# Kernel optimization log

Measured on AMD Instinct MI355X. Metric: run time of the kernel, lower is better.

The kernel has to match this reference:

```python
import jax, jax.numpy as jnp
import numpy as np

N = 100000      # nodes
E = 1600000     # directed edges
F_IN = 128      # node feature dim
H = 128         # hidden dim
C = 16          # classes


def setup_inputs() -> dict:
    key = jax.random.key(0)
    ks = jax.random.split(key, 8)
    s = 1.0 / np.sqrt(H)
    return {
        "x": jax.random.normal(ks[0], (N, F_IN), dtype=jnp.float32),
        "edge_index": jax.random.randint(ks[1], (2, E), 0, N, dtype=jnp.int32),
        "W1": jax.random.normal(ks[2], (F_IN, H), dtype=jnp.float32) * s,
        "b1": jnp.zeros((H,), jnp.float32),
        "W2": jax.random.normal(ks[3], (H, H), dtype=jnp.float32) * s,
        "b2": jnp.zeros((H,), jnp.float32),
        "W3": jax.random.normal(ks[4], (H, H), dtype=jnp.float32) * s,
        "b3": jnp.zeros((H,), jnp.float32),
        "Wfc": jax.random.normal(ks[5], (H, C), dtype=jnp.float32) * s,
        "bfc": jnp.zeros((C,), jnp.float32),
    }


def _gcn_conv(x, W, b, src, dst, norm):
    # x' = b + scatter_add over edges of norm * (x @ W)[src] into dst
    h = x @ W                                   # [N, H] dense GEMM
    msg = h[src] * norm[:, None]                # [E+N, H] gather + scale
    out = jax.ops.segment_sum(msg, dst, num_segments=N)  # scatter-add
    return out + b


def reference(x, edge_index, W1, b1, W2, b2, W3, b3, Wfc, bfc):
    loops = jnp.arange(N, dtype=edge_index.dtype)
    src = jnp.concatenate([edge_index[0], loops])   # [E+N] with self-loops
    dst = jnp.concatenate([edge_index[1], loops])
    # symmetric normalization deg^{-1/2}[src] * deg^{-1/2}[dst] (PyG default)
    deg = jax.ops.segment_sum(jnp.ones_like(dst, dtype=x.dtype), dst, num_segments=N)
    dinv = jax.lax.rsqrt(deg)                       # deg >= 1 due to self-loops
    norm = dinv[src] * dinv[dst]

    h = jax.nn.elu(_gcn_conv(x, W1, b1, src, dst, norm))   # dropout is identity in eval
    h = jax.nn.elu(_gcn_conv(h, W2, b2, src, dst, norm))
    h = jax.nn.elu(_gcn_conv(h, W3, b3, src, dst, norm))
    logits = h @ Wfc + bfc                                  # [N, C]
    return jax.nn.log_softmax(logits, axis=-1)
```

## Files before the change

kernel.cpp:

```cpp
#include <hip/hip_runtime.h>
#include <math.h>

#define HDIM 128
#define CDIM 16
#define CAP 48
#define ASTR 136
#define HSTR 132
#define NBINS 256
#define TILE 4096
#define NPBMAX 512
#define SORTCAP 7424

typedef unsigned short u16;
typedef unsigned int u32;
typedef __attribute__((ext_vector_type(8))) short short8;
typedef __attribute__((ext_vector_type(4))) float f32x4;
typedef __attribute__((ext_vector_type(2))) float f32x2;

__device__ inline u16 f2bf(float f) {
  u32 u = __float_as_uint(f);
  u += 0x7fffu + ((u >> 16) & 1u);
  return (u16)(u >> 16);
}
__device__ inline float bf_lo(u32 p) { return __uint_as_float(p << 16); }
__device__ inline float bf_hi(u32 p) { return __uint_as_float(p & 0xffff0000u); }
__device__ inline u32 cvtpk(float a, float b) {
  u32 r;
  asm("v_cvt_pk_bf16_f32 %0, %1, %2" : "=v"(r) : "v"(a), "v"(b));
  return r;
}
__device__ inline void acc_word(f32x2& acc, u32 w) {
  f32x2 x;
  x.x = __uint_as_float(w << 16);
  x.y = __uint_as_float(w & 0xffff0000u);
  asm("v_pk_add_f32 %0, %1, %2" : "=v"(acc) : "v"(x), "v"(acc));
}


__global__ __launch_bounds__(256) void bin_kernel(const int* __restrict__ ei,
                                                  int* __restrict__ cursor,
                                                  u32* __restrict__ bins,
                                                  int binCap, int E, int npb, int nbE,
                                                  int nbW, int N,
                                                  const float* __restrict__ W0,
                                                  const float* __restrict__ W1,
                                                  const float* __restrict__ W2,
                                                  u16* __restrict__ Wt,
                                                  u16* __restrict__ Arow,
                                                  u16* __restrict__ Brow,
                                                  u16* __restrict__ Xrow) {
  int tid = threadIdx.x;
  if (blockIdx.x >= nbE) {
    if (blockIdx.x >= nbE + nbW) {
      if (tid < 16) ((uint4*)Arow)[tid] = make_uint4(0, 0, 0, 0);
      else if (tid < 32) ((uint4*)Brow)[tid - 16] = make_uint4(0, 0, 0, 0);
      else if (tid < 48) ((uint4*)Xrow)[tid - 32] = make_uint4(0, 0, 0, 0);
      return;
    }
    int t = (blockIdx.x - nbE) * 256 + tid;
    int which = t >> 14, idx = t & 16383;
    int n = idx >> 7, k = idx & 127;
    const float* W = which == 0 ? W0 : (which == 1 ? W1 : W2);
    Wt[(size_t)which * HDIM * HDIM + n * HDIM + k] = f2bf(W[k * HDIM + n]);
    return;
  }
  __shared__ u32 eds32[TILE];
  __shared__ u32 srt[TILE];
  __shared__ unsigned char bid[TILE];
  __shared__ int hist[NBINS], lbase[NBINS + 1], gbase[NBINS], rnk[NBINS];
  int t0 = blockIdx.x * TILE;
  int n = min(TILE, E - t0);
  hist[tid] = 0;
  rnk[tid] = 0;
  __syncthreads();
  for (int i = tid; i < n; i += 256) {
    int s = ei[t0 + i];
    int d = ei[E + t0 + i];
    int b = d / npb;
    eds32[i] = ((u32)(d - b * npb) << 17) | (u32)s;
    bid[i] = (unsigned char)b;
    atomicAdd(&hist[b], 1);
  }
  __syncthreads();
  int h = hist[tid];
  lbase[tid] = h;
  __syncthreads();
#pragma unroll
  for (int off = 1; off < 256; off <<= 1) {
    int v = tid >= off ? lbase[tid - off] : 0;
    __syncthreads();
    lbase[tid] += v;
    __syncthreads();
  }
  int ex = lbase[tid] - h;
  __syncthreads();
  lbase[tid] = ex;
  if (tid == 255) lbase[256] = ex + h;
  gbase[tid] = h ? atomicAdd(&cursor[tid], h) : 0;
  __syncthreads();
  for (int i = tid; i < n; i += 256) {
    int b = bid[i];
    int r = lbase[b] + atomicAdd(&rnk[b], 1);
    srt[r] = eds32[i];
  }
  __syncthreads();
  for (int i = tid; i < n; i += 256) {
    int lo = 0, hi = 255;
#pragma unroll
    for (int k = 0; k < 8; ++k) {
      int mid = (lo + hi + 1) >> 1;
      if (lbase[mid] <= i) lo = mid; else hi = mid - 1;
    }
    int r = gbase[lo] + (i - lbase[lo]);
    if (r < binCap) bins[(size_t)lo * binCap + r] = srt[i];
  }
}

__global__ __launch_bounds__(256) void fill2_kernel(const u32* __restrict__ bins,
                                                    const int* __restrict__ cursor,
                                                    int binCap, int npb,
                                                    int* __restrict__ deg,
                                                    int* __restrict__ csr, int N) {
  __shared__ int hist[NPBMAX];
  __shared__ int base[NPBMAX + 1];
  __shared__ int sorted[SORTCAP];
  int b = blockIdx.x;
  int tid = threadIdx.x;
  int n0 = b * npb;
  int nn = min(npb, N - n0);
  if (nn <= 0) return;
  int cnt = min(min(cursor[b], binCap), SORTCAP);
  const u32* eb = bins + (size_t)b * binCap;
  for (int i = tid; i < nn; i += 256) hist[i] = 0;
  __syncthreads();
  for (int i = tid; i < cnt; i += 256) atomicAdd(&hist[eb[i] >> 17], 1);
  __syncthreads();
  if (tid == 0) {
    int s = 0;
    for (int i = 0; i < nn; ++i) { base[i] = s; s += hist[i]; }
    base[nn] = s;
  }
  __syncthreads();
  for (int i = tid; i < nn; i += 256) hist[i] = 0;
  __syncthreads();
  for (int i = tid; i < cnt; i += 256) {
    u32 w = eb[i];
    int loc = w >> 17;
    sorted[base[loc] + atomicAdd(&hist[loc], 1)] = (int)(w & 0x1FFFFu);
  }
  __syncthreads();
  for (int i = tid; i < nn; i += 256) deg[n0 + i] = base[i + 1] - base[i];
  int total = nn * CAP;
  int* cout = csr + (size_t)n0 * CAP;
  for (int i = tid; i < total; i += 256) {
    int loc = (int)(((u32)(i >> 4) * 21846u) >> 16);
    int j = i - loc * CAP;
    int s0 = base[loc];
    int dc = min(base[loc + 1] - s0, CAP);
    cout[i] = j < dc ? sorted[s0 + j] : N;
  }
}

__global__ __launch_bounds__(256) void convert_k(const float* __restrict__ x,
                                                 const int* __restrict__ deg,
                                                 u16* __restrict__ Xc, int N) {
  int rg = blockIdx.x * 64 + (threadIdx.x >> 2);
  if (rg >= N) return;
  int c = threadIdx.x & 3;
  float dv = rsqrtf((float)(deg[rg] + 1));
  const float4* src = (const float4*)(x + (size_t)rg * HDIM + c * 32);
  uint4* dst = (uint4*)(Xc + (size_t)rg * HDIM + c * 32);
#pragma unroll
  for (int j = 0; j < 4; ++j) {
    float4 a = src[2 * j], b = src[2 * j + 1];
    uint4 o;
    o.x = cvtpk(dv * a.x, dv * a.y); o.y = cvtpk(dv * a.z, dv * a.w);
    o.z = cvtpk(dv * b.x, dv * b.y); o.w = cvtpk(dv * b.z, dv * b.w);
    dst[j] = o;
  }
}


__device__ inline void gather16(const u16* __restrict__ G, const int* __restrict__ deg,
                                const int* __restrict__ csr, int node, int l, float* v) {
  const char* Gb = (const char*)G;
  f32x2 p0, p1, p2, p3;
  {
    uint4 sr = *(const uint4*)(Gb + ((size_t)node << 8) + (l << 4));
    p0.x = bf_lo(sr.x); p0.y = bf_hi(sr.x);
    p1.x = bf_lo(sr.y); p1.y = bf_hi(sr.y);
    p2.x = bf_lo(sr.z); p2.y = bf_hi(sr.z);
    p3.x = bf_lo(sr.w); p3.y = bf_hi(sr.w);
  }
  int dfull = deg[node];
  int d = min(dfull, CAP);
  int dp = (d + 7) & ~7;
  const int* row = csr + (size_t)node * CAP;
  int i0 = row[l];
  int i1 = d > 16 ? row[16 + l] : 0;
  int i2 = d > 32 ? row[32 + l] : 0;

#define GLD(u) (*(const uint4*)(Gb + (((u32)(u)) << 8) + (l << 4)))
#define AW(gv) { acc_word(p0, gv.x); acc_word(p1, gv.y); acc_word(p2, gv.z); acc_word(p3, gv.w); }
  for (int k = 0; k < dp; k += 8) {
    int s = k < 16 ? i0 : (k < 32 ? i1 : i2);
    int bl = k & 15;
    int u0 = __shfl(s, bl + 0, 16), u1 = __shfl(s, bl + 1, 16);
    int u2 = __shfl(s, bl + 2, 16), u3 = __shfl(s, bl + 3, 16);
    int u4 = __shfl(s, bl + 4, 16), u5 = __shfl(s, bl + 5, 16);
    int u6 = __shfl(s, bl + 6, 16), u7 = __shfl(s, bl + 7, 16);
    uint4 g0 = GLD(u0), g1 = GLD(u1), g2 = GLD(u2), g3 = GLD(u3);
    uint4 g4 = GLD(u4), g5 = GLD(u5), g6 = GLD(u6), g7 = GLD(u7);
    AW(g0) AW(g1) AW(g2) AW(g3) AW(g4) AW(g5) AW(g6) AW(g7)
  }
#undef AW
#undef GLD
  float dvn = rsqrtf((float)(dfull + 1));
  v[0] = dvn * p0.x; v[1] = dvn * p0.y;
  v[2] = dvn * p1.x; v[3] = dvn * p1.y;
  v[4] = dvn * p2.x; v[5] = dvn * p2.y;
  v[6] = dvn * p3.x; v[7] = dvn * p3.y;
}


__global__ __launch_bounds__(256) void agg_gemm(const u16* __restrict__ G,
                                                const int* __restrict__ deg,
                                                const int* __restrict__ csr,
                                                const float* __restrict__ b,
                                                const u16* __restrict__ Wn,
                                                u16* __restrict__ Gout, int N) {
  __shared__ u16 As[16 * ASTR];
  __shared__ float dvs[16];
  int tid = threadIdx.x;
  int node0 = blockIdx.x * 16;
  int lr = tid >> 4, l = tid & 15;
  int node = node0 + lr;
  if (tid < 16) dvs[tid] = rsqrtf((float)(deg[min(node0 + tid, N - 1)] + 1));
  if (node < N) {
    float v[8];
    gather16(G, deg, csr, node, l, v);
    uint4 o;
    o.x = cvtpk(v[0], v[1]); o.y = cvtpk(v[2], v[3]);
    o.z = cvtpk(v[4], v[5]); o.w = cvtpk(v[6], v[7]);
    *(uint4*)(As + lr * ASTR + l * 8) = o;
  } else {
    *(uint4*)(As + lr * ASTR + l * 8) = make_uint4(0, 0, 0, 0);
  }
  __syncthreads();

  int w = tid >> 6;
  int lw = tid & 63;
  int m = lw & 15, q = lw >> 4;
  f32x4 acc0 = (f32x4){0.f, 0.f, 0.f, 0.f};
  f32x4 acc1 = (f32x4){0.f, 0.f, 0.f, 0.f};
#pragma unroll
  for (int kc = 0; kc < 4; ++kc) {
    short8 af = *(const short8*)(As + m * ASTR + kc * 32 + q * 8);
    short8 b0 = *(const short8*)(Wn + ((w * 2 + 0) * 16 + m) * HDIM + kc * 32 + q * 8);
    short8 b1 = *(const short8*)(Wn + ((w * 2 + 1) * 16 + m) * HDIM + kc * 32 + q * 8);
    acc0 = __builtin_amdgcn_mfma_f32_16x16x32_bf16(af, b0, acc0, 0, 0, 0);
    acc1 = __builtin_amdgcn_mfma_f32_16x16x32_bf16(af, b1, acc1, 0, 0, 0);
  }
  __syncthreads();

  float bc0 = b[(w * 2 + 0) * 16 + m], bc1 = b[(w * 2 + 1) * 16 + m];
#pragma unroll
  for (int r = 0; r < 4; ++r) {
    float dvr = dvs[q * 4 + r];
    float h0 = acc0[r] + bc0; h0 = h0 > 0.f ? h0 : __expf(h0) - 1.f;
    float h1 = acc1[r] + bc1; h1 = h1 > 0.f ? h1 : __expf(h1) - 1.f;
    As[(q * 4 + r) * ASTR + (w * 2 + 0) * 16 + m] = f2bf(h0 * dvr);
    As[(q * 4 + r) * ASTR + (w * 2 + 1) * 16 + m] = f2bf(h1 * dvr);
  }
  __syncthreads();

  {
    int r = tid >> 4, c = tid & 15;
    if (node0 + r < N)
      *(uint4*)(Gout + (size_t)(node0 + r) * HDIM + c * 8) =
          *(const uint4*)(As + r * ASTR + c * 8);
  }
}


__global__ __launch_bounds__(256) void agg_fc(const u16* __restrict__ G,
                                              const int* __restrict__ deg,
                                              const int* __restrict__ csr,
                                              const float* __restrict__ b3,
                                              const u16* __restrict__ W3t,
                                              const float* __restrict__ Wfc,
                                              const float* __restrict__ bfc,
                                              float* __restrict__ out, int N) {
  __shared__ u16 As[16 * ASTR];
  __shared__ float Hs[16 * HSTR];
  __shared__ float Wl[HDIM * CDIM];
  int tid = threadIdx.x;
  for (int i = tid; i < HDIM * CDIM; i += 256) Wl[i] = Wfc[i];

  int node0 = blockIdx.x * 16;
  int lr = tid >> 4, l = tid & 15;
  int node = node0 + lr;
  if (node < N) {
    float v[8];
    gather16(G, deg, csr, node, l, v);
    uint4 o;
    o.x = cvtpk(v[0], v[1]); o.y = cvtpk(v[2], v[3]);
    o.z = cvtpk(v[4], v[5]); o.w = cvtpk(v[6], v[7]);
    *(uint4*)(As + lr * ASTR + l * 8) = o;
  } else {
    *(uint4*)(As + lr * ASTR + l * 8) = make_uint4(0, 0, 0, 0);
  }
  __syncthreads();

  int w = tid >> 6;
  int lw = tid & 63;
  int m = lw & 15, q = lw >> 4;
  f32x4 acc0 = (f32x4){0.f, 0.f, 0.f, 0.f};
  f32x4 acc1 = (f32x4){0.f, 0.f, 0.f, 0.f};
#pragma unroll
  for (int kc = 0; kc < 4; ++kc) {
    short8 af = *(const short8*)(As + m * ASTR + kc * 32 + q * 8);
    short8 w0 = *(const short8*)(W3t + ((w * 2 + 0) * 16 + m) * HDIM + kc * 32 + q * 8);
    short8 w1 = *(const short8*)(W3t + ((w * 2 + 1) * 16 + m) * HDIM + kc * 32 + q * 8);
    acc0 = __builtin_amdgcn_mfma_f32_16x16x32_bf16(af, w0, acc0, 0, 0, 0);
    acc1 = __builtin_amdgcn_mfma_f32_16x16x32_bf16(af, w1, acc1, 0, 0, 0);
  }
  float bc0 = b3[(w * 2 + 0) * 16 + m], bc1 = b3[(w * 2 + 1) * 16 + m];
#pragma unroll
  for (int r = 0; r < 4; ++r) {
    float h0 = acc0[r] + bc0; h0 = h0 > 0.f ? h0 : __expf(h0) - 1.f;
    float h1 = acc1[r] + bc1; h1 = h1 > 0.f ? h1 : __expf(h1) - 1.f;
    Hs[(q * 4 + r) * HSTR + (w * 2 + 0) * 16 + m] = h0;
    Hs[(q * 4 + r) * HSTR + (w * 2 + 1) * 16 + m] = h1;
  }
  __syncthreads();

  int rg = node0 + lr;
  if (rg >= N) return;
  int c = l;
  const float* hrow = Hs + lr * HSTR;
  float acc = bfc[c];
#pragma unroll 4
  for (int k4 = 0; k4 < 32; ++k4) {
    float4 g = *(const float4*)(hrow + k4 * 4);
    const float* wk = Wl + (k4 * 4) * CDIM + c;
    acc = fmaf(g.x, wk[0 * CDIM], acc);
    acc = fmaf(g.y, wk[1 * CDIM], acc);
    acc = fmaf(g.z, wk[2 * CDIM], acc);
    acc = fmaf(g.w, wk[3 * CDIM], acc);
  }
  float mx = acc;
  for (int off = 8; off >= 1; off >>= 1) mx = fmaxf(mx, __shfl_xor(mx, off, 16));
  float ex = __expf(acc - mx);
  float ssum = ex;
  for (int off = 8; off >= 1; off >>= 1) ssum += __shfl_xor(ssum, off, 16);
  out[(size_t)rg * CDIM + c] = (acc - mx) - __logf(ssum);
}


extern "C" void kernel_launch(void* const* d_in, const int* in_sizes, int n_in,
                              void* d_out, int out_size, void* d_ws, size_t ws_size,
                              hipStream_t stream) {
  const float* x   = (const float*)d_in[0];
  const int*   ei  = (const int*)d_in[1];
  const float* W1  = (const float*)d_in[2];
  const float* b1  = (const float*)d_in[3];
  const float* W2  = (const float*)d_in[4];
  const float* b2  = (const float*)d_in[5];
  const float* W3  = (const float*)d_in[6];
  const float* b3  = (const float*)d_in[7];
  const float* Wfc = (const float*)d_in[8];
  const float* bfc = (const float*)d_in[9];

  const int N = in_sizes[0] / HDIM;
  const int E = in_sizes[1] / 2;
  const int npb = (N + NBINS - 1) / NBINS;
  const int binCap = (E + NBINS - 1) / NBINS + 1024;
  const int nbE = (E + TILE - 1) / TILE;
  const int nbW = 3 * HDIM * HDIM / 256;

  char* ws = (char*)d_ws;
  size_t off = 0;
  auto alloc = [&](size_t bytes) -> void* {
    void* p = ws + off;
    off += (bytes + 511) & ~(size_t)511;
    return p;
  };
  int*   deg    = (int*)alloc((size_t)N * 4);
  int*   cursor = (int*)alloc((size_t)NBINS * 4);
  int*   csr    = (int*)alloc((size_t)N * CAP * 4);
  u32*   bins   = (u32*)alloc((size_t)NBINS * binCap * 4);
  u16*   Wt     = (u16*)alloc((size_t)3 * HDIM * HDIM * 2);
  u16*   Xc     = (u16*)alloc((size_t)(N + 1) * HDIM * 2);
  u16*   A      = (u16*)alloc((size_t)(N + 1) * HDIM * 2);
  u16*   B      = (u16*)alloc((size_t)(N + 1) * HDIM * 2);

  hipMemsetAsync(cursor, 0, (size_t)NBINS * 4, stream);
  bin_kernel<<<nbE + nbW + 1, 256, 0, stream>>>(ei, cursor, bins, binCap, E, npb, nbE, nbW,
                                                N, W1, W2, W3, Wt,
                                                A + (size_t)N * HDIM, B + (size_t)N * HDIM,
                                                Xc + (size_t)N * HDIM);
  fill2_kernel<<<NBINS, 256, 0, stream>>>(bins, cursor, binCap, npb, deg, csr, N);
  convert_k<<<(N + 63) / 64, 256, 0, stream>>>(x, deg, Xc, N);

  int grid16 = (N + 15) / 16;
  agg_gemm<<<grid16, 256, 0, stream>>>(Xc, deg, csr, b1, Wt, A, N);
  agg_gemm<<<grid16, 256, 0, stream>>>(A, deg, csr, b2, Wt + HDIM * HDIM, B, N);
  agg_fc<<<grid16, 256, 0, stream>>>(B, deg, csr, b3, Wt + 2 * HDIM * HDIM, Wfc, bfc,
                                     (float*)d_out, N);
}
```

Measured before the change: 369.4 us.

## Split fill kernel into half-bin blocks and fuse feature conversion into it

The CSR fill kernel now launches two blocks per destination bin, each handling half the bin's nodes. It replaces the serial thread-0 prefix sum with a wave-shuffle scan and uses smaller shared arrays, which should raise occupancy. The separate convert kernel is folded into the fill kernel, saving a launch and reading degrees from shared memory. Each half-block still scans the whole bin's edge list, so edge reads double. TILE also drops to 2048, which changes the binning setup.

```diff
diff --git a/kernel.cpp b/kernel.cpp
--- a/kernel.cpp
+++ b/kernel.cpp
@@ -7,9 +7,8 @@
 #define ASTR 136
 #define HSTR 132
 #define NBINS 256
-#define TILE 4096
-#define NPBMAX 512
-#define SORTCAP 7424
+#define TILE 2048
+#define SORTCAP2 3968
 
 typedef unsigned short u16;
 typedef unsigned int u32;
@@ -120,63 +119,94 @@
                                                     const int* __restrict__ cursor,
                                                     int binCap, int npb,
                                                     int* __restrict__ deg,
-                                                    int* __restrict__ csr, int N) {
-  __shared__ int hist[NPBMAX];
-  __shared__ int base[NPBMAX + 1];
-  __shared__ int sorted[SORTCAP];
-  int b = blockIdx.x;
+                                                    int* __restrict__ csr, int N,
+                                                    const float* __restrict__ x,
+                                                    u16* __restrict__ Xc) {
+  __shared__ int hist[256];
+  __shared__ int base[257];
+  __shared__ int wsum[4], wpre[4];
+  __shared__ int sorted[SORTCAP2];
   int tid = threadIdx.x;
-  int n0 = b * npb;
-  int nn = min(npb, N - n0);
-  if (nn <= 0) return;
-  int cnt = min(min(cursor[b], binCap), SORTCAP);
+  int half = (npb + 1) >> 1;
+  int b = blockIdx.x >> 1, part = blockIdx.x & 1;
+  int n0b = b * npb;
+  int nnb = min(npb, N - n0b);
+  if (nnb <= 0) return;
+  int h0 = part * half;
+  int hn = min(half, nnb - h0);
+  if (hn <= 0) return;
+  int n0 = n0b + h0;
+  int cnt = min(cursor[b], binCap);
   const u32* eb = bins + (size_t)b * binCap;
-  for (int i = tid; i < nn; i += 256) hist[i] = 0;
-  __syncthreads();
-  for (int i = tid; i < cnt; i += 256) atomicAdd(&hist[eb[i] >> 17], 1);
-  __syncthreads();
-  if (tid == 0) {
-    int s = 0;
-    for (int i = 0; i < nn; ++i) { base[i] = s; s += hist[i]; }
-    base[nn] = s;
-  }
-  __syncthreads();
-  for (int i = tid; i < nn; i += 256) hist[i] = 0;
+
+  hist[tid] = 0;
+  __syncthreads();
+  for (int i = tid; i < cnt; i += 256) {
+    int loc = (int)(eb[i] >> 17) - h0;
+    if ((u32)loc < (u32)hn) atomicAdd(&hist[loc], 1);
+  }
+  __syncthreads();
+  int h = hist[tid];
+  {
+    int lane = tid & 63, wid = tid >> 6;
+    int v = h;
+#pragma unroll
+    for (int off = 1; off < 64; off <<= 1) {
+      int o = __shfl_up(v, off, 64);
+      if (lane >= off) v += o;
+    }
+    if (lane == 63) wsum[wid] = v;
+    __syncthreads();
+    if (tid == 0) {
+      int s = 0;
+#pragma unroll
+      for (int w = 0; w < 4; ++w) { wpre[w] = s; s += wsum[w]; }
+    }
+    __syncthreads();
+    base[tid + 1] = v + wpre[wid];
+    if (tid == 0) base[0] = 0;
+  }
+  __syncthreads();
+  if (tid < hn) deg[n0 + tid] = h;
+  hist[tid] = 0;
   __syncthreads();
   for (int i = tid; i < cnt; i += 256) {
     u32 w = eb[i];
-    int loc = w >> 17;
-    sorted[base[loc] + atomicAdd(&hist[loc], 1)] = (int)(w & 0x1FFFFu);
-  }
-  __syncthreads();
-  for (int i = tid; i < nn; i += 256) deg[n0 + i] = base[i + 1] - base[i];
-  int total = nn * CAP;
-  int* cout = csr + (size_t)n0 * CAP;
-  for (int i = tid; i < total; i += 256) {
-    int loc = (int)(((u32)(i >> 4) * 21846u) >> 16);
-    int j = i - loc * CAP;
-    int s0 = base[loc];
-    int dc = min(base[loc + 1] - s0, CAP);
-    cout[i] = j < dc ? sorted[s0 + j] : N;
-  }
-}
-
-__global__ __launch_bounds__(256) void convert_k(const float* __restrict__ x,
-                                                 const int* __restrict__ deg,
-                                                 u16* __restrict__ Xc, int N) {
-  int rg = blockIdx.x * 64 + (threadIdx.x >> 2);
-  if (rg >= N) return;
-  int c = threadIdx.x & 3;
-  float dv = rsqrtf((float)(deg[rg] + 1));
-  const float4* src = (const float4*)(x + (size_t)rg * HDIM + c * 32);
-  uint4* dst = (uint4*)(Xc + (size_t)rg * HDIM + c * 32);
-#pragma unroll
-  for (int j = 0; j < 4; ++j) {
-    float4 a = src[2 * j], b = src[2 * j + 1];
-    uint4 o;
-    o.x = cvtpk(dv * a.x, dv * a.y); o.y = cvtpk(dv * a.z, dv * a.w);
-    o.z = cvtpk(dv * b.x, dv * b.y); o.w = cvtpk(dv * b.z, dv * b.w);
-    dst[j] = o;
+    int loc = (int)(w >> 17) - h0;
+    if ((u32)loc < (u32)hn) {
+      int p = base[loc] + atomicAdd(&hist[loc], 1);
+      if (p < SORTCAP2) sorted[p] = (int)(w & 0x1FFFFu);
+    }
+  }
+  __syncthreads();
+  {
+    int total = hn * CAP;
+    int* cout = csr + (size_t)n0 * CAP;
+    for (int i = tid; i < total; i += 256) {
+      int loc = (int)(((u32)(i >> 4) * 21846u) >> 16);
+      int j = i - loc * CAP;
+      int s0 = base[loc];
+      int dc = min(base[loc + 1] - s0, CAP);
+      int idx = s0 + j;
+      cout[i] = (j < dc && idx < SORTCAP2) ? sorted[idx] : N;
+    }
+  }
+  {
+    int c = tid & 3;
+    for (int rr = tid >> 2; rr < hn; rr += 64) {
+      int rg = n0 + rr;
+      float dv = rsqrtf((float)(base[rr + 1] - base[rr] + 1));
+      const float4* src = (const float4*)(x + (size_t)rg * HDIM + c * 32);
+      uint4* dst = (uint4*)(Xc + (size_t)rg * HDIM + c * 32);
+#pragma unroll
+      for (int j = 0; j < 4; ++j) {
+        float4 a = src[2 * j], bb = src[2 * j + 1];
+        uint4 o;
+        o.x = cvtpk(dv * a.x, dv * a.y); o.y = cvtpk(dv * a.z, dv * a.w);
+        o.z = cvtpk(dv * bb.x, dv * bb.y); o.w = cvtpk(dv * bb.z, dv * bb.w);
+        dst[j] = o;
+      }
+    }
   }
 }
 
@@ -400,8 +430,7 @@
                                                 N, W1, W2, W3, Wt,
                                                 A + (size_t)N * HDIM, B + (size_t)N * HDIM,
                                                 Xc + (size_t)N * HDIM);
-  fill2_kernel<<<NBINS, 256, 0, stream>>>(bins, cursor, binCap, npb, deg, csr, N);
-  convert_k<<<(N + 63) / 64, 256, 0, stream>>>(x, deg, Xc, N);
+  fill2_kernel<<<NBINS * 2, 256, 0, stream>>>(bins, cursor, binCap, npb, deg, csr, N, x, Xc);
 
   int grid16 = (N + 15) / 16;
   agg_gemm<<<grid16, 256, 0, stream>>>(Xc, deg, csr, b1, Wt, A, N);
```

New measurement: 364.8 us. Within noise of the previous version (-1.2%).
